# Kernel tuning notes

Measured on AMD Instinct MI355X. Metric: run time of the kernel, lower is better.

The kernel has to match this reference:

```python
import jax, jax.numpy as jnp
import numpy as np

N = 65536          # total atoms
M = 12             # max neighbors
ORIG = 92          # orig_atom_fea_len
NBR = 41           # nbr_fea_len
AF = 64            # atom_fea_len
NCONV = 3
HF = 128           # h_fea_len
N0 = 1024          # number of crystals
EPS = 1e-5


def _glorot(key, shape):
    fan_in, fan_out = shape[0], shape[-1]
    lim = np.sqrt(6.0 / (fan_in + fan_out)).astype(np.float32)
    return jax.random.uniform(key, shape, jnp.float32, -lim, lim)


def setup_inputs() -> dict:
    key = jax.random.key(0)
    ks = jax.random.split(key, 16)
    atom_fea = jax.random.normal(ks[0], (N, ORIG), jnp.float32)
    nbr_fea = jax.random.normal(ks[1], (N, M, NBR), jnp.float32)
    nbr_fea_idx = jax.random.randint(ks[2], (N, M), 0, N, jnp.int32)
    # flat segment ids: ~64 atoms per crystal, contiguous (mimics ragged idx lists)
    crystal_idx = jnp.repeat(jnp.arange(N0, dtype=jnp.int32), N // N0)
    # parameters
    emb_w = _glorot(ks[3], (ORIG, AF)); emb_b = jnp.zeros((AF,), jnp.float32)
    conv_fc_w = _glorot(ks[4], (NCONV, 2 * AF + NBR, 2 * AF))
    conv_fc_b = jnp.zeros((NCONV, 2 * AF), jnp.float32)
    conv_bn1_g = jnp.ones((NCONV, 2 * AF), jnp.float32)
    conv_bn1_b = jnp.zeros((NCONV, 2 * AF), jnp.float32)
    conv_bn2_g = jnp.ones((NCONV, AF), jnp.float32)
    conv_bn2_b = jnp.zeros((NCONV, AF), jnp.float32)
    fc1_w = _glorot(ks[5], (AF, HF)); fc1_b = jnp.zeros((HF,), jnp.float32)
    out1_w = _glorot(ks[6], (HF, HF // 2)); out1_b = jnp.zeros((HF // 2,), jnp.float32)
    out2_w = _glorot(ks[7], (HF // 2, 1)); out2_b = jnp.zeros((1,), jnp.float32)
    return dict(atom_fea=atom_fea, nbr_fea=nbr_fea, nbr_fea_idx=nbr_fea_idx,
                crystal_idx=crystal_idx, emb_w=emb_w, emb_b=emb_b,
                conv_fc_w=conv_fc_w, conv_fc_b=conv_fc_b,
                conv_bn1_g=conv_bn1_g, conv_bn1_b=conv_bn1_b,
                conv_bn2_g=conv_bn2_g, conv_bn2_b=conv_bn2_b,
                fc1_w=fc1_w, fc1_b=fc1_b, out1_w=out1_w, out1_b=out1_b,
                out2_w=out2_w, out2_b=out2_b)


def _batchnorm(x, g, b):
    # training-mode BatchNorm1d over axis 0, biased variance, eps=1e-5
    mu = jnp.mean(x, axis=0)
    var = jnp.var(x, axis=0)
    return (x - mu) * jax.lax.rsqrt(var + EPS) * g + b


def _conv_layer(afea, nbr_fea, nbr_idx, w, b, g1, b1, g2, b2):
    # gather neighbor atom features: (N, M, AF)
    atom_nbr = afea[nbr_idx]
    self_fea = jnp.broadcast_to(afea[:, None, :], (N, M, AF))
    total = jnp.concatenate([self_fea, atom_nbr, nbr_fea], axis=-1)  # (N, M, 2AF+NBR)
    gated = jnp.einsum('nmf,fg->nmg', total, w) + b                  # (N, M, 2AF)
    gated = _batchnorm(gated.reshape(-1, 2 * AF), g1, b1).reshape(N, M, 2 * AF)
    filt, core = jnp.split(gated, 2, axis=-1)
    nbr_sumed = jnp.sum(jax.nn.sigmoid(filt) * jax.nn.softplus(core), axis=1)  # scatter-sum over nbrs
    nbr_sumed = _batchnorm(nbr_sumed, g2, b2)
    return jax.nn.softplus(afea + nbr_sumed)


def reference(atom_fea, nbr_fea, nbr_fea_idx, crystal_idx, emb_w, emb_b,
              conv_fc_w, conv_fc_b, conv_bn1_g, conv_bn1_b, conv_bn2_g, conv_bn2_b,
              fc1_w, fc1_b, out1_w, out1_b, out2_w, out2_b):
    afea = atom_fea @ emb_w + emb_b                 # (N, AF)
    identity = afea
    for i in range(NCONV):
        afea = _conv_layer(afea, nbr_fea, nbr_fea_idx,
                           conv_fc_w[i], conv_fc_b[i],
                           conv_bn1_g[i], conv_bn1_b[i],
                           conv_bn2_g[i], conv_bn2_b[i])
        afea = afea + identity
        identity = afea
    # ragged per-crystal mean pooling via segment_sum
    sums = jax.ops.segment_sum(afea, crystal_idx, num_segments=N0)
    counts = jax.ops.segment_sum(jnp.ones((N,), afea.dtype), crystal_idx, num_segments=N0)
    crys = sums / jnp.maximum(counts, 1.0)[:, None]  # (N0, AF)
    crys = jax.nn.softplus(crys) @ fc1_w + fc1_b
    crys = jax.nn.softplus(crys)                     # (N0, HF) == repr
    out = jax.nn.softplus(crys @ out1_w + out1_b) @ out2_w + out2_b  # (N0, 1)
    return out, crys
```

## Files before the change

kernel.cpp:

```cpp
#include <hip/hip_runtime.h>

#define NATOM 65536
#define MNBR 12
#define NMROW (NATOM*MNBR)
#define ORIG 92
#define NBRF 41
#define AF 64
#define HF 128
#define NCRYS 1024
#define EPSBN 1e-5f
#define NBP 48
#define CGRID 2048
#define NTASK 16384

typedef __attribute__((ext_vector_type(8))) short short8;
typedef __attribute__((ext_vector_type(4))) float floatx4;

__device__ __forceinline__ float softplusf_(float x){
    return fmaxf(x,0.f) + __logf(1.f + __expf(-fabsf(x)));
}
__device__ __forceinline__ float sigmoidf_(float x){
    return __builtin_amdgcn_rcpf(1.f + __expf(-x));
}
__device__ __forceinline__ short f2bf(float x){
    unsigned u = __float_as_uint(x);
    u += 0x7fffu + ((u >> 16) & 1u);
    return (short)(u >> 16);
}
__device__ __forceinline__ unsigned packbf(float f, float g){
    return (unsigned)(unsigned short)f2bf(f) | ((unsigned)(unsigned short)f2bf(g) << 16);
}

__global__ void k_embed(const float* __restrict__ atom_fea, const float* __restrict__ emb_w,
                        const float* __restrict__ emb_b, float* __restrict__ afea,
                        short* __restrict__ abf)
{
    __shared__ float wl[ORIG*AF];
    __shared__ float bl[AF];
    __shared__ float rows[4*ORIG];
    int tid = threadIdx.x;
    for (int i = tid; i < ORIG*AF; i += 256) wl[i] = emb_w[i];
    if (tid < AF) bl[tid] = emb_b[tid];
    __syncthreads();
    for (int t = blockIdx.x; t < NATOM/4; t += gridDim.x) {
        for (int i = tid; i < 4*ORIG; i += 256) rows[i] = atom_fea[t*4*ORIG + i];
        __syncthreads();
        int r = tid >> 6, c = tid & 63;
        float acc = bl[c];
        const float* rp = &rows[r*ORIG];
        #pragma unroll 4
        for (int k = 0; k < ORIG; ++k) acc += rp[k] * wl[k*AF + c];
        int n = t*4 + r;
        afea[n*AF + c] = acc;
        abf[n*AF + c] = f2bf(acc);
        __syncthreads();
    }
}

__global__ void k_prep_nbr(const float* __restrict__ nbr_fea, short* __restrict__ nbf)
{
    int g = blockIdx.x*256 + threadIdx.x;
    int row = g / 6, c = g % 6;
    const float* src = nbr_fea + (long)row*NBRF + c*8;
    short8 v = {0,0,0,0,0,0,0,0};
    if (c < 5) {
        #pragma unroll
        for (int j = 0; j < 8; ++j) v[j] = f2bf(__builtin_nontemporal_load(src + j));
    } else {
        v[0] = f2bf(__builtin_nontemporal_load(src));
    }
    *(short8*)(nbf + (long)g*8) = v;
}

__global__ void k_prep_w(const float* __restrict__ W, short* __restrict__ wt2)
{
    int g = blockIdx.x*256 + threadIdx.x;
    int j = g & 7, c = (g >> 3) & 127, q = (g >> 10) & 3, ks = g >> 12;
    int k = ks*32 + q*8 + j;
    wt2[g] = (k < 169) ? f2bf(W[k*128 + c]) : (short)0;
}

template<int MODE>
__global__ __launch_bounds__(256, 3)
void k_conv(const short* __restrict__ abf, const short* __restrict__ nbf,
            const int* __restrict__ nbr_idx, const short* __restrict__ wt2,
            const float* __restrict__ bias,
            float* __restrict__ stats1, const float* __restrict__ bn1ss,
            float* __restrict__ nsum, float* __restrict__ stats2,
            unsigned* __restrict__ gpair)
{
    __shared__ __align__(16) short stg[2][6432];
    __shared__ float pbuf[(MODE==1) ? 4*12*17 : 4];

    int tid = threadIdx.x;
    int lane = tid & 63, wave = tid >> 6;
    int l15 = lane & 15, q = lane >> 4;
    int cf = wave*16 + l15;
    int cc = 64 + cf;

    short8 wf[6][2];
    #pragma unroll
    for (int ks = 0; ks < 6; ++ks) {
        wf[ks][0] = *(const short8*)(wt2 + ((ks*4+q)*128 + cf)*8);
        wf[ks][1] = *(const short8*)(wt2 + ((ks*4+q)*128 + cc)*8);
    }
    float bs0 = bias[cf], bs1 = bias[cc];
    float sc0=0.f, sh0=0.f, sc1=0.f, sh1=0.f;
    if (MODE==1) { sc0=bn1ss[cf]; sh0=bn1ss[128+cf]; sc1=bn1ss[cc]; sh1=bn1ss[128+cc]; }

    int kind[3], ldso[3], nrow[3]; long gco[3];
    #pragma unroll
    for (int s = 0; s < 3; ++s) {
        int i = tid + s*256;
        if (i < 384)      { kind[s]=0; int row=i>>3, c=i&7; nrow[s]=row; ldso[s]=row*72+c*8; gco[s]=c*8; }
        else if (i < 672) { kind[s]=1; int j=i-384; int row=j/6, c=j%6; nrow[s]=0; ldso[s]=3456+row*56+c*8; gco[s]=row*48+c*8; }
        else if (i < 704) { kind[s]=2; int j=i-672; int a=j>>3, c=j&7; nrow[s]=0; ldso[s]=6144+a*72+c*8; gco[s]=a*64+c*8; }
        else              { kind[s]=3; nrow[s]=0; ldso[s]=0; gco[s]=0; }
    }
    int art[3], nvo[3], evo[3], svo[3];
    #pragma unroll
    for (int rt = 0; rt < 3; ++rt) {
        int r = rt*16 + l15;
        art[rt] = r/12;
        nvo[rt] = r*72 + q*8;
        evo[rt] = 3456 + r*56 + q*8;
        svo[rt] = 6144 + art[rt]*72 + q*8;
    }

    float s_acc[2]={0.f,0.f}, s2_acc[2]={0.f,0.f};
    float st2s = 0.f, st2q = 0.f;
    const short8 zf = {0,0,0,0,0,0,0,0};
    float* pb = pbuf + ((MODE==1) ? wave*(12*17) : 0);
    const int bt = blockIdx.x;

    int nid[3];
    short8 hold[3];
    #pragma unroll
    for (int s = 0; s < 3; ++s)
        if (kind[s]==0) nid[s] = nbr_idx[bt*48 + nrow[s]];
    #pragma unroll
    for (int s = 0; s < 3; ++s) {
        if (kind[s]==0)      hold[s] = *(const short8*)(abf + (unsigned)nid[s]*64u + gco[s]);
        else if (kind[s]==1) hold[s] = *(const short8*)(nbf + (long)bt*2304 + gco[s]);
        else if (kind[s]==2) hold[s] = *(const short8*)(abf + (unsigned)bt*256u + gco[s]);
    }
    #pragma unroll
    for (int s = 0; s < 3; ++s)
        if (kind[s]==0) nid[s] = nbr_idx[(bt+CGRID)*48 + nrow[s]];
    #pragma unroll
    for (int s = 0; s < 3; ++s)
        if (kind[s] < 3) *(short8*)(&stg[0][0] + ldso[s]) = hold[s];
    __syncthreads();

    #pragma unroll 2
    for (int k = 0; k < 8; ++k) {
        int b = bt + k*CGRID;
        if (k < 7) {
            int bn = b + CGRID;
            #pragma unroll
            for (int s = 0; s < 3; ++s) {
                if (kind[s]==0)      hold[s] = *(const short8*)(abf + (unsigned)nid[s]*64u + gco[s]);
                else if (kind[s]==1) hold[s] = *(const short8*)(nbf + (long)bn*2304 + gco[s]);
                else if (kind[s]==2) hold[s] = *(const short8*)(abf + (unsigned)bn*256u + gco[s]);
            }
            if (k < 6) {
                #pragma unroll
                for (int s = 0; s < 3; ++s)
                    if (kind[s]==0) nid[s] = nbr_idx[(bn+CGRID)*48 + nrow[s]];
            }
        }

        const short* sb = &stg[k & 1][0];
        floatx4 acc[3][2];
        #pragma unroll
        for (int rt=0; rt<3; ++rt) {
            acc[rt][0] = (floatx4){bs0,bs0,bs0,bs0};
            acc[rt][1] = (floatx4){bs1,bs1,bs1,bs1};
        }
        #pragma unroll
        for (int rt = 0; rt < 3; ++rt) {
            short8 sv0 = *(const short8*)(sb + svo[rt]);
            short8 sv1 = *(const short8*)(sb + svo[rt] + 32);
            short8 nv0 = *(const short8*)(sb + nvo[rt]);
            short8 nv1 = *(const short8*)(sb + nvo[rt] + 32);
            short8 ev0 = *(const short8*)(sb + evo[rt]);
            short8 ev1 = (q < 2) ? *(const short8*)(sb + evo[rt] + 32) : zf;
            #pragma unroll
            for (int ct = 0; ct < 2; ++ct) {
                acc[rt][ct] = __builtin_amdgcn_mfma_f32_16x16x32_bf16(sv0, wf[0][ct], acc[rt][ct], 0,0,0);
                acc[rt][ct] = __builtin_amdgcn_mfma_f32_16x16x32_bf16(sv1, wf[1][ct], acc[rt][ct], 0,0,0);
                acc[rt][ct] = __builtin_amdgcn_mfma_f32_16x16x32_bf16(nv0, wf[2][ct], acc[rt][ct], 0,0,0);
                acc[rt][ct] = __builtin_amdgcn_mfma_f32_16x16x32_bf16(nv1, wf[3][ct], acc[rt][ct], 0,0,0);
                acc[rt][ct] = __builtin_amdgcn_mfma_f32_16x16x32_bf16(ev0, wf[4][ct], acc[rt][ct], 0,0,0);
                acc[rt][ct] = __builtin_amdgcn_mfma_f32_16x16x32_bf16(ev1, wf[5][ct], acc[rt][ct], 0,0,0);
            }
        }

        if (MODE != 1) {
            #pragma unroll
            for (int ct=0; ct<2; ++ct)
                #pragma unroll
                for (int rt=0; rt<3; ++rt)
                    #pragma unroll
                    for (int r=0; r<4; ++r) {
                        float v = acc[rt][ct][r];
                        s_acc[ct] += v; s2_acc[ct] += v*v;
                    }
        }
        if (MODE == 2) {
            #pragma unroll
            for (int rt=0; rt<3; ++rt) {
                unsigned base = (unsigned)(b*48 + rt*16 + q*4)*64u + (unsigned)(wave*16 + l15);
                #pragma unroll
                for (int r=0; r<4; ++r)
                    __builtin_nontemporal_store(packbf(acc[rt][0][r], acc[rt][1][r]),
                                                gpair + base + (unsigned)r*64u);
            }
        }
        if (MODE == 1) {
            #pragma unroll
            for (int rt=0; rt<3; ++rt) {
                float part = 0.f;
                #pragma unroll
                for (int r=0; r<4; ++r) {
                    float f = acc[rt][0][r]*sc0 + sh0;
                    float g = acc[rt][1][r]*sc1 + sh1;
                    part += sigmoidf_(f) * softplusf_(g);
                }
                pb[(rt*4+q)*17 + l15] = part;
            }
            int a = lane >> 4, c16 = lane & 15;
            float s = pb[(3*a+0)*17 + c16] + pb[(3*a+1)*17 + c16] + pb[(3*a+2)*17 + c16];
            nsum[(b*4 + a)*AF + wave*16 + c16] = s;
            st2s += s; st2q += s*s;
        }

        if (k < 7) {
            short* db = &stg[(k + 1) & 1][0];
            #pragma unroll
            for (int s = 0; s < 3; ++s)
                if (kind[s] < 3) *(short8*)(db + ldso[s]) = hold[s];
        }
        __syncthreads();
    }

    if (MODE != 1) {
        #pragma unroll
        for (int ct=0; ct<2; ++ct) {
            float s = s_acc[ct], s2 = s2_acc[ct];
            s  += __shfl_xor(s, 16);  s  += __shfl_xor(s, 32);
            s2 += __shfl_xor(s2, 16); s2 += __shfl_xor(s2, 32);
            if (q == 0) {
                int c = ct ? cc : cf;
                atomicAdd(&stats1[c], s);
                atomicAdd(&stats1[128 + c], s2);
            }
        }
    } else {
        st2s += __shfl_xor(st2s, 16); st2s += __shfl_xor(st2s, 32);
        st2q += __shfl_xor(st2q, 16); st2q += __shfl_xor(st2q, 32);
        if (q == 0) {
            atomicAdd(&stats2[cf], st2s);
            atomicAdd(&stats2[64 + cf], st2q);
        }
    }
}

__global__ __launch_bounds__(256, 4)
void k_gate(const unsigned* __restrict__ gpair, const float* __restrict__ stats1,
            const float* __restrict__ g1, const float* __restrict__ b1,
            float* __restrict__ nsum, float* __restrict__ stats2)
{
    __shared__ float red[2][4][64];
    int tid = threadIdx.x;
    int lane = tid & 63, wave = tid >> 6;
    float mf = stats1[lane]       * (1.f/NMROW);
    float vf = stats1[128+lane]   * (1.f/NMROW) - mf*mf;
    float scf = g1[lane] * rsqrtf(vf + EPSBN);
    float shf = b1[lane] - mf*scf;
    float mc = stats1[64+lane]    * (1.f/NMROW);
    float vc = stats1[192+lane]   * (1.f/NMROW) - mc*mc;
    float scc = g1[64+lane] * rsqrtf(vc + EPSBN);
    float shc = b1[64+lane] - mc*scc;
    float st2s = 0.f, st2q = 0.f;
    int a0 = blockIdx.x*64 + wave;
    for (int j = 0; j < 16; ++j) {
        int atom = a0 + j*4;
        const unsigned* gp = gpair + (unsigned)atom*12u*64u + lane;
        unsigned u[12];
        #pragma unroll
        for (int i = 0; i < 12; ++i) u[i] = __builtin_nontemporal_load(gp + i*64);
        float s = 0.f;
        #pragma unroll
        for (int i = 0; i < 12; ++i) {
            float f = __uint_as_float(u[i] << 16);
            float g = __uint_as_float(u[i] & 0xffff0000u);
            f = f*scf + shf;
            g = g*scc + shc;
            s += sigmoidf_(f) * softplusf_(g);
        }
        nsum[atom*AF + lane] = s;
        st2s += s; st2q += s*s;
    }
    red[0][wave][lane] = st2s;
    red[1][wave][lane] = st2q;
    __syncthreads();
    if (tid < 64) {
        float s  = red[0][0][tid] + red[0][1][tid] + red[0][2][tid] + red[0][3][tid];
        float s2 = red[1][0][tid] + red[1][1][tid] + red[1][2][tid] + red[1][3][tid];
        atomicAdd(&stats2[tid], s);
        atomicAdd(&stats2[64 + tid], s2);
    }
}

__global__ void k_bn1fin(const float* __restrict__ stats1, const float* __restrict__ g,
                         const float* __restrict__ b, float* __restrict__ bn1ss)
{
    int c = threadIdx.x;
    float mean = stats1[c] * (1.f/NMROW);
    float var  = stats1[128+c] * (1.f/NMROW) - mean*mean;
    float scale = g[c] * rsqrtf(var + EPSBN);
    bn1ss[c] = scale;
    bn1ss[128+c] = b[c] - mean*scale;
}

__global__ void k_update(float* __restrict__ afea, short* __restrict__ abf,
                         const float* __restrict__ nsum,
                         const float* __restrict__ stats2,
                         const float* __restrict__ g2, const float* __restrict__ b2)
{
    int g = blockIdx.x*256 + threadIdx.x;
    int c = g & 63;
    float mean = stats2[c] * (1.f/NATOM);
    float var  = stats2[64+c] * (1.f/NATOM) - mean*mean;
    float scale = g2[c]*rsqrtf(var + EPSBN);
    float shift = b2[c] - mean*scale;
    float ns = nsum[g]*scale + shift;
    float a = afea[g];
    float v = softplusf_(a + ns) + a;
    afea[g] = v; abf[g] = f2bf(v);
}

__global__ void k_pool(const float* __restrict__ afea, const int* __restrict__ cidx,
                       float* __restrict__ pool, float* __restrict__ cnt)
{
    int g = blockIdx.x*256 + threadIdx.x;
    int c = g & 63; int chunk = g >> 6;
    float run = 0.f, rc = 0.f; int cur = -1;
    for (int i = 0; i < 16; ++i) {
        int a = chunk*16 + i;
        int cr = cidx[a];
        float v = afea[a*64 + c];
        if (cr != cur) {
            if (cur >= 0) { atomicAdd(&pool[cur*64+c], run); if (c==0) atomicAdd(&cnt[cur], rc); }
            run = 0.f; rc = 0.f; cur = cr;
        }
        run += v; rc += 1.f;
    }
    atomicAdd(&pool[cur*64+c], run); if (c==0) atomicAdd(&cnt[cur], rc);
}

__global__ void k_head(const float* __restrict__ pool, const float* __restrict__ cnt,
                       const float* __restrict__ fc1w, const float* __restrict__ fc1b,
                       const float* __restrict__ o1w, const float* __restrict__ o1b,
                       const float* __restrict__ o2w, const float* __restrict__ o2b,
                       float* __restrict__ dout)
{
    __shared__ float spv[64], crys[128], h1[64];
    int b = blockIdx.x, tid = threadIdx.x;
    if (tid < 64) {
        float ct = fmaxf(cnt[b], 1.f);
        spv[tid] = softplusf_(pool[b*64+tid] / ct);
    }
    __syncthreads();
    float a = fc1b[tid];
    for (int k = 0; k < 64; ++k) a += spv[k] * fc1w[k*128 + tid];
    float v = softplusf_(a);
    crys[tid] = v;
    dout[NCRYS + b*128 + tid] = v;
    __syncthreads();
    if (tid < 64) {
        float a2 = o1b[tid];
        for (int k = 0; k < 128; ++k) a2 += crys[k] * o1w[k*64 + tid];
        h1[tid] = softplusf_(a2) * o2w[tid];
    }
    __syncthreads();
    if (tid == 0) {
        float s = o2b[0];
        for (int j = 0; j < 64; ++j) s += h1[j];
        dout[b] = s;
    }
}

extern "C" void kernel_launch(void* const* d_in, const int* in_sizes, int n_in,
                              void* d_out, int out_size, void* d_ws, size_t ws_size,
                              hipStream_t stream)
{
    const float* atom_fea = (const float*)d_in[0];
    const float* nbr_fea  = (const float*)d_in[1];
    const int*   nbr_idx  = (const int*)d_in[2];
    const int*   cidx     = (const int*)d_in[3];
    const float* emb_w    = (const float*)d_in[4];
    const float* emb_b    = (const float*)d_in[5];
    const float* cfw      = (const float*)d_in[6];
    const float* cfb      = (const float*)d_in[7];
    const float* bn1g     = (const float*)d_in[8];
    const float* bn1b     = (const float*)d_in[9];
    const float* bn2g     = (const float*)d_in[10];
    const float* bn2b     = (const float*)d_in[11];
    const float* fc1w     = (const float*)d_in[12];
    const float* fc1b     = (const float*)d_in[13];
    const float* o1w      = (const float*)d_in[14];
    const float* o1b      = (const float*)d_in[15];
    const float* o2w      = (const float*)d_in[16];
    const float* o2b      = (const float*)d_in[17];

    float* ws    = (float*)d_ws;
    float* afea  = ws;
    float* nsum  = ws + 4194304;
    short* abf   = (short*)(ws + 8388608);
    short* nbf   = (short*)(ws + 10485760);
    short* wt2   = (short*)(ws + 29360128);
    float* stats = ws + 29372416;
    float* pool  = ws + 29374336;
    float* cnt   = ws + 29439872;
    unsigned* gpair = (unsigned*)(ws + 29440896);

    bool big = ws_size >= (size_t)(29440896 + 50331648) * 4;

    hipMemsetAsync(stats, 0, (1920 + 65536 + 1024)*sizeof(float), stream);

    k_prep_nbr<<<(NMROW*6)/256, 256, 0, stream>>>(nbr_fea, nbf);
    k_embed<<<2048, 256, 0, stream>>>(atom_fea, emb_w, emb_b, afea, abf);

    for (int L = 0; L < 3; ++L) {
        float* st1 = stats + L*640;
        float* ss  = st1 + 256;
        float* st2 = st1 + 512;
        k_prep_w<<<96, 256, 0, stream>>>(cfw + L*169*128, wt2);
        if (big) {
            k_conv<2><<<CGRID, 256, 0, stream>>>(abf, nbf, nbr_idx, wt2, cfb + L*128,
                                                 st1, nullptr, nullptr, nullptr, gpair);
            k_gate<<<NATOM/64, 256, 0, stream>>>(gpair, st1, bn1g + L*128, bn1b + L*128,
                                                 nsum, st2);
        } else {
            k_conv<0><<<CGRID, 256, 0, stream>>>(abf, nbf, nbr_idx, wt2, cfb + L*128,
                                                 st1, nullptr, nullptr, nullptr, nullptr);
            k_bn1fin<<<1, 128, 0, stream>>>(st1, bn1g + L*128, bn1b + L*128, ss);
            k_conv<1><<<CGRID, 256, 0, stream>>>(abf, nbf, nbr_idx, wt2, cfb + L*128,
                                                 nullptr, ss, nsum, st2, nullptr);
        }
        k_update<<<16384, 256, 0, stream>>>(afea, abf, nsum, st2, bn2g + L*64, bn2b + L*64);
    }
    k_pool<<<1024, 256, 0, stream>>>(afea, cidx, pool, cnt);
    k_head<<<NCRYS, 128, 0, stream>>>(pool, cnt, fc1w, fc1b, o1w, o1b, o2w, o2b, (float*)d_out);
}
```

Measured before the change: 821.8 us.

## Deepen conv gather prefetch to two tiles ahead and raise occupancy

```diff
diff --git a/kernel.cpp b/kernel.cpp
--- a/kernel.cpp
+++ b/kernel.cpp
@@ -81,7 +81,7 @@
 }
 
 template<int MODE>
-__global__ __launch_bounds__(256, 3)
+__global__ __launch_bounds__(256, 4)
 void k_conv(const short* __restrict__ abf, const short* __restrict__ nbf,
             const int* __restrict__ nbr_idx, const short* __restrict__ wt2,
             const float* __restrict__ bias,
@@ -108,7 +108,7 @@
     float sc0=0.f, sh0=0.f, sc1=0.f, sh1=0.f;
     if (MODE==1) { sc0=bn1ss[cf]; sh0=bn1ss[128+cf]; sc1=bn1ss[cc]; sh1=bn1ss[128+cc]; }
 
-    int kind[3], ldso[3], nrow[3]; long gco[3];
+    int kind[3], ldso[3], nrow[3], gco[3];
     #pragma unroll
     for (int s = 0; s < 3; ++s) {
         int i = tid + s*256;
@@ -133,41 +133,55 @@
     float* pb = pbuf + ((MODE==1) ? wave*(12*17) : 0);
     const int bt = blockIdx.x;
 
-    int nid[3];
-    short8 hold[3];
+    int nidb[2][3];
+    short8 hold[2][3];
+
     #pragma unroll
     for (int s = 0; s < 3; ++s)
-        if (kind[s]==0) nid[s] = nbr_idx[bt*48 + nrow[s]];
+        if (kind[s]==0) nidb[0][s] = nbr_idx[bt*48 + nrow[s]];
+    short8 h0[3];
     #pragma unroll
     for (int s = 0; s < 3; ++s) {
-        if (kind[s]==0)      hold[s] = *(const short8*)(abf + (unsigned)nid[s]*64u + gco[s]);
-        else if (kind[s]==1) hold[s] = *(const short8*)(nbf + (long)bt*2304 + gco[s]);
-        else if (kind[s]==2) hold[s] = *(const short8*)(abf + (unsigned)bt*256u + gco[s]);
+        if (kind[s]==0)      h0[s] = *(const short8*)(abf + (unsigned)nidb[0][s]*64u + gco[s]);
+        else if (kind[s]==1) h0[s] = *(const short8*)(nbf + (unsigned)bt*2304u + gco[s]);
+        else if (kind[s]==2) h0[s] = *(const short8*)(abf + (unsigned)bt*256u + gco[s]);
     }
     #pragma unroll
     for (int s = 0; s < 3; ++s)
-        if (kind[s]==0) nid[s] = nbr_idx[(bt+CGRID)*48 + nrow[s]];
+        if (kind[s]==0) nidb[1][s] = nbr_idx[(bt+CGRID)*48 + nrow[s]];
     #pragma unroll
     for (int s = 0; s < 3; ++s)
-        if (kind[s] < 3) *(short8*)(&stg[0][0] + ldso[s]) = hold[s];
+        if (kind[s] < 3) *(short8*)(&stg[0][0] + ldso[s]) = h0[s];
+    {
+        unsigned bn = (unsigned)(bt + CGRID);
+        #pragma unroll
+        for (int s = 0; s < 3; ++s) {
+            if (kind[s]==0)      hold[1][s] = *(const short8*)(abf + (unsigned)nidb[1][s]*64u + gco[s]);
+            else if (kind[s]==1) hold[1][s] = *(const short8*)(nbf + bn*2304u + gco[s]);
+            else if (kind[s]==2) hold[1][s] = *(const short8*)(abf + bn*256u + gco[s]);
+        }
+    }
+    #pragma unroll
+    for (int s = 0; s < 3; ++s)
+        if (kind[s]==0) nidb[0][s] = nbr_idx[(bt+2*CGRID)*48 + nrow[s]];
     __syncthreads();
 
     #pragma unroll 2
     for (int k = 0; k < 8; ++k) {
         int b = bt + k*CGRID;
-        if (k < 7) {
-            int bn = b + CGRID;
+        if (k < 6) {
+            unsigned bn = (unsigned)(b + 2*CGRID);
             #pragma unroll
             for (int s = 0; s < 3; ++s) {
-                if (kind[s]==0)      hold[s] = *(const short8*)(abf + (unsigned)nid[s]*64u + gco[s]);
-                else if (kind[s]==1) hold[s] = *(const short8*)(nbf + (long)bn*2304 + gco[s]);
-                else if (kind[s]==2) hold[s] = *(const short8*)(abf + (unsigned)bn*256u + gco[s]);
+                if (kind[s]==0)      hold[k&1][s] = *(const short8*)(abf + (unsigned)nidb[k&1][s]*64u + gco[s]);
+                else if (kind[s]==1) hold[k&1][s] = *(const short8*)(nbf + bn*2304u + gco[s]);
+                else if (kind[s]==2) hold[k&1][s] = *(const short8*)(abf + bn*256u + gco[s]);
             }
-            if (k < 6) {
-                #pragma unroll
-                for (int s = 0; s < 3; ++s)
-                    if (kind[s]==0) nid[s] = nbr_idx[(bn+CGRID)*48 + nrow[s]];
-            }
+        }
+        if (k < 5) {
+            #pragma unroll
+            for (int s = 0; s < 3; ++s)
+                if (kind[s]==0) nidb[(k+1)&1][s] = nbr_idx[(b+3*CGRID)*48 + nrow[s]];
         }
 
         const short* sb = &stg[k & 1][0];
@@ -213,8 +227,7 @@
                 unsigned base = (unsigned)(b*48 + rt*16 + q*4)*64u + (unsigned)(wave*16 + l15);
                 #pragma unroll
                 for (int r=0; r<4; ++r)
-                    __builtin_nontemporal_store(packbf(acc[rt][0][r], acc[rt][1][r]),
-                                                gpair + base + (unsigned)r*64u);
+                    gpair[base + (unsigned)r*64u] = packbf(acc[rt][0][r], acc[rt][1][r]);
             }
         }
         if (MODE == 1) {
@@ -239,7 +252,7 @@
             short* db = &stg[(k + 1) & 1][0];
             #pragma unroll
             for (int s = 0; s < 3; ++s)
-                if (kind[s] < 3) *(short8*)(db + ldso[s]) = hold[s];
+                if (kind[s] < 3) *(short8*)(db + ldso[s]) = hold[(k+1)&1][s];
         }
         __syncthreads();
     }
@@ -289,7 +302,7 @@
         const unsigned* gp = gpair + (unsigned)atom*12u*64u + lane;
         unsigned u[12];
         #pragma unroll
-        for (int i = 0; i < 12; ++i) u[i] = __builtin_nontemporal_load(gp + i*64);
+        for (int i = 0; i < 12; ++i) u[i] = gp[i*64];
         float s = 0.f;
         #pragma unroll
         for (int i = 0; i < 12; ++i) {
```

Measured after the change: 1.388 ms. 1.69x slower.
